# Performance work log

Measured on AMD Instinct MI355X. Metric: run time of the kernel, lower is better.

The kernel has to match this reference:

```python
import jax, jax.numpy as jnp
import numpy as np
from jax.scipy.special import erf, digamma, i0

B, L, D, H = 4, 4096, 512, 4
_MAX_SQRT_GRADIENT = 1000.0

@jax.custom_vjp
def sqrt_bound(x):
    return jnp.sqrt(x)

def _sb_fwd(x):
    return jnp.sqrt(x), x

def _sb_bwd(x, g):
    return (g / jnp.sqrt(jnp.clip(4.0 * x, 1.0 / _MAX_SQRT_GRADIENT**2, None)),)

sqrt_bound.defvjp(_sb_fwd, _sb_bwd)

def block_diag_linear(x, w):
    # x: [..., D], w: [h, bw, bw] block-diagonal weight
    h, bw, _ = w.shape
    xr = x.reshape(x.shape[:-1] + (h, bw))
    return jnp.einsum('...hi,hij->...hj', xr, w).reshape(x.shape)

def self_att_pool(x, num_heads):
    n_state = x.shape[-1] // num_heads
    attn = jax.nn.softmax(jnp.einsum('bld,bmd->blm', x, x) / np.float32(np.sqrt(n_state)), axis=-1)
    # max over the sequence axis of the attended values, keepdims -> [B,1,D]
    return jnp.max(jnp.einsum('blm,bmd->bld', attn, x), axis=-2, keepdims=True)

def ripple_transform_hybrid(t, mix_params):
    mix = jax.nn.softmax(mix_params)
    return mix[0] * digamma(t + 1.0) + mix[1] * i0(t)

def ripple_act(data, alpha, beta, mix_params, temperature=1.0):
    def f(d):
        norm = erf(d / (jnp.max(d) * alpha))
        return jnp.sum(ripple_transform_hybrid(norm * beta, mix_params))
    g = jnp.clip(jax.grad(f)(data), -1.0, 1.0)
    return jax.nn.softmax(-g / temperature, axis=-1)  # softmin

def ripplemoe_act(data, weights, alphas, beta, mix_params, temperature=1.0):
    def f(d):
        dmax = jnp.max(d)
        norm = erf(d[None] / (dmax * alphas[:, None, None]))  # [S,B,L]
        t = ripple_transform_hybrid(norm * beta, mix_params)
        w = jax.nn.softmax(weights)
        return jnp.sum(w[:, None, None] * t)
    g = jnp.clip(jax.grad(f)(data), -1.0, 1.0)
    return jax.nn.softmax(-g / temperature, axis=-1)  # softmin

def token_selection(x, cls_w, cls_b, token_weights, prelu_a, ts_weights, ts_alphas, ts_beta, ts_mix):
    scores = jnp.einsum('bld,sd->sbl', x, cls_w) + cls_b[:, None, None]  # [S,B,L]
    p = jnp.where(scores >= 0, scores, prelu_a * scores)  # PReLU
    ts = jax.nn.celu(p) * jax.nn.silu(p) + jax.nn.gelu(p, approximate=False)
    combined = jnp.einsum('s,sbl->bl', jax.nn.selu(token_weights[:, 0]), ts)
    _, idx = jax.lax.top_k(combined, combined.shape[-1])  # k = L, descending permutation
    vals = ts.sum(0)  # [B,L]
    b_idx = jnp.arange(combined.shape[0])[:, None]
    importance = jnp.ones_like(combined).at[b_idx, idx].add(vals)
    return (1.0 + ripplemoe_act(importance, ts_weights, ts_alphas, ts_beta, ts_mix))[..., None]

def _forward(x, attention_space, W_spatial, W_sil, W_ohead, W_out, w_ig, w_ag, a_param,
             cls_w, cls_b, token_weights, prelu_a, ts_weights, ts_alphas, ts_beta, ts_mix,
             pa1_alpha, pa1_beta, pa1_mix, pa2_alpha, pa2_beta, pa2_mix):
    spatial = jnp.einsum('bld,de->ble', x, attention_space) @ W_spatial.T
    # RG-LRU style gating
    gate_x = jax.nn.sigmoid(block_diag_linear(x, w_ig))
    gate_a = jax.nn.sigmoid(block_diag_linear(x, w_ag))
    log_a = -8.0 * jax.nn.softplus(a_param) * gate_a
    normalized_x = x * gate_x * sqrt_bound(1.0 - jnp.exp(2.0 * log_a))
    gated = jnp.exp(log_a) * self_att_pool(spatial, H) + normalized_x
    sparsity = ripple_act(gated @ W_sil.T, pa1_alpha, pa1_beta, pa1_mix)
    attn = (gated * sparsity) @ W_ohead.T
    sel = token_selection(x, cls_w, cls_b, token_weights, prelu_a, ts_weights, ts_alphas, ts_beta, ts_mix)
    out = ripple_act(attn * sel, pa2_alpha, pa2_beta, pa2_mix)
    return out @ W_out.T

def setup_inputs() -> dict:
    key = jax.random.key(0)
    ks = jax.random.split(key, 12)
    lim = float(1.0 / np.sqrt(D))
    xav = float(np.sqrt(6.0 / (2 * D)))
    bw = D // H
    u = jax.random.uniform(ks[8], (D,), jnp.float32, 0.9**2 + 1e-8, 0.999**2 + 1e-8)
    return {
        'x': jax.random.normal(ks[0], (B, L, D), jnp.float32),
        'attention_space': jax.random.uniform(ks[1], (D, D), jnp.float32, -xav, xav),
        'W_spatial': jax.random.uniform(ks[2], (D, D), jnp.float32, -lim, lim),
        'W_sil': jax.random.uniform(ks[3], (D, D), jnp.float32, -lim, lim),
        'W_ohead': jax.random.uniform(ks[4], (D, D), jnp.float32, -lim, lim),
        'W_out': jax.random.uniform(ks[5], (D, D), jnp.float32, -lim, lim),
        'w_ig': jax.random.normal(ks[6], (H, bw, bw), jnp.float32) * np.float32(np.sqrt(1.0 / bw)),
        'w_ag': jax.random.normal(ks[7], (H, bw, bw), jnp.float32) * np.float32(np.sqrt(1.0 / bw)),
        'a_param': jnp.log(jnp.exp(-0.5 * jnp.log(u)) - 1.0),
        'cls_w': jax.random.uniform(ks[9], (H, D), jnp.float32, -lim, lim),
        'cls_b': jax.random.uniform(ks[10], (H,), jnp.float32, -lim, lim),
        'token_weights': jax.random.normal(ks[11], (H, 1), jnp.float32),
        'prelu_a': jnp.array(0.25, jnp.float32),
        'ts_weights': jnp.ones(H, jnp.float32) / H,
        'ts_alphas': jnp.ones(H, jnp.float32),
        'ts_beta': jnp.array(1.0, jnp.float32),
        'ts_mix': jnp.full((2,), 0.5, jnp.float32),
        'pa1_alpha': jnp.array(1.0, jnp.float32),
        'pa1_beta': jnp.array(1.0, jnp.float32),
        'pa1_mix': jnp.full((2,), 0.5, jnp.float32),
        'pa2_alpha': jnp.array(1.0, jnp.float32),
        'pa2_beta': jnp.array(1.0, jnp.float32),
        'pa2_mix': jnp.full((2,), 0.5, jnp.float32),
    }

def reference(x, attention_space, W_spatial, W_sil, W_ohead, W_out, w_ig, w_ag, a_param,
              cls_w, cls_b, token_weights, prelu_a, ts_weights, ts_alphas, ts_beta, ts_mix,
              pa1_alpha, pa1_beta, pa1_mix, pa2_alpha, pa2_beta, pa2_mix):
    return _forward(x, attention_space, W_spatial, W_sil, W_ohead, W_out, w_ig, w_ag, a_param,
                    cls_w, cls_b, token_weights, prelu_a, ts_weights, ts_alphas, ts_beta, ts_mix,
                    pa1_alpha, pa1_beta, pa1_mix, pa2_alpha, pa2_beta, pa2_mix)
```

## Files before the change

kernel.cpp:

```cpp
#include <hip/hip_runtime.h>

typedef unsigned short ushort;
typedef unsigned int uint;
typedef unsigned long long u64;

#define DEV __device__ __forceinline__

typedef __attribute__((ext_vector_type(4))) float f32x4;
typedef __bf16 bf16x8 __attribute__((ext_vector_type(8)));
typedef __attribute__((ext_vector_type(4))) ushort u16x4;
typedef __attribute__((ext_vector_type(8))) ushort u16x8;

static constexpr int B_ = 4, L_ = 4096, D_ = 512;
static constexpr long NE = (long)B_ * L_ * D_;

DEV float b2f(ushort u) { return __uint_as_float(((uint)u) << 16); }
DEV ushort f2b(float f) {
    uint u = __float_as_uint(f);
    uint r = u + 0x7FFFu + ((u >> 16) & 1u);
    return (ushort)(r >> 16);
}
DEV uint mapF(float f) {
    uint b = __float_as_uint(f);
    return (b & 0x80000000u) ? ~b : (b | 0x80000000u);
}
DEV float unmapF(uint u) {
    uint b = (u & 0x80000000u) ? (u & 0x7FFFFFFFu) : ~u;
    return __uint_as_float(b);
}
DEV float rcp_(float x) { return __builtin_amdgcn_rcpf(x); }
DEV float fexp(float x) { return __builtin_amdgcn_exp2f(x * 1.44269504089f); }
DEV float sigm(float x) { return rcp_(1.f + fexp(-x)); }

DEV void gload16(const ushort* g, ushort* l) {
    __builtin_amdgcn_global_load_lds((const __attribute__((address_space(1))) void*)g,
                                     (__attribute__((address_space(3))) void*)l, 16, 0, 0);
}

DEV int xcd_swz(int b, int nwg) {
    int q = nwg >> 3, r = nwg & 7;
    int x = b & 7, i = b >> 3;
    int base = (x < r) ? x * (q + 1) : r * (q + 1) + (x - r) * q;
    return base + i;
}

DEV float trigamma1p(float t) {
    float x = t + 1.f;
    float acc = 0.f;
#pragma unroll
    for (int k = 0; k < 6; k++) { float xx = x + (float)k; acc += rcp_(xx * xx); }
    float y = x + 6.f;
    float iy = rcp_(y), iy2 = iy * iy;
    return acc + iy * (1.f + iy * (0.5f + iy * (0.166666667f + iy2 * (-0.0333333333f + iy2 * 0.0238095238f))));
}
DEV float besselI1(float t) {
    float q = 0.25f * t * t;
    return 0.5f * t * (1.f + q * (0.5f + q * (0.0833333333f + q * (0.00694444444f + q * (3.47222222e-4f + q * 1.15740741e-5f)))));
}
DEV float rippleH(float u, float beta, float mix0, float mix1) {
    float t = beta * erff(u);
    float Tp = mix0 * trigamma1p(t) + mix1 * besselI1(t);
    float ep = 1.12837917f * fexp(-u * u);
    return beta * Tp * ep;
}

DEV void gemm_core(const ushort* __restrict__ A, int lda,
                   const ushort* __restrict__ Bt, int ldb, int K,
                   ushort* __restrict__ Alds, ushort* __restrict__ Blds,
                   f32x4 (&acc)[4][4])
{
    const int tid = threadIdx.x;
    const int lane = tid & 63;
    const int wave = tid >> 6;
    const int wr = wave >> 1, wc = wave & 1;

    const int srow = wave * 16 + (lane >> 2);
    const int skc = (lane & 3) * 8;
    const ushort* Ag0 = A + (size_t)srow * lda + skc;
    const ushort* Ag1 = A + (size_t)(srow + 64) * lda + skc;
    const ushort* Bg0 = Bt + (size_t)srow * ldb + skc;
    const ushort* Bg1 = Bt + (size_t)(srow + 64) * ldb + skc;
    const int wb = wave * 512;

    const int ar = wr * 64 + (lane & 15);
    const int br = wc * 64 + (lane & 15);
    const int kk = (lane >> 4) * 8;

    gload16(Ag0, Alds + wb);
    gload16(Ag1, Alds + 2048 + wb);
    gload16(Bg0, Blds + wb);
    gload16(Bg1, Blds + 2048 + wb);
    __syncthreads();

    int cur = 0;
    for (int k0 = 0; k0 < K; k0 += 32) {
        const int nb = cur ^ 1;
        if (k0 + 32 < K) {
            gload16(Ag0 + k0 + 32, Alds + nb * 4096 + wb);
            gload16(Ag1 + k0 + 32, Alds + nb * 4096 + 2048 + wb);
            gload16(Bg0 + k0 + 32, Blds + nb * 4096 + wb);
            gload16(Bg1 + k0 + 32, Blds + nb * 4096 + 2048 + wb);
        }
        bf16x8 af[4], bfr[4];
#pragma unroll
        for (int mi = 0; mi < 4; mi++) af[mi] = *(const bf16x8*)&Alds[cur * 4096 + (ar + mi * 16) * 32 + kk];
#pragma unroll
        for (int ni = 0; ni < 4; ni++) bfr[ni] = *(const bf16x8*)&Blds[cur * 4096 + (br + ni * 16) * 32 + kk];
#pragma unroll
        for (int mi = 0; mi < 4; mi++)
#pragma unroll
            for (int ni = 0; ni < 4; ni++)
                acc[mi][ni] = __builtin_amdgcn_mfma_f32_16x16x32_bf16(af[mi], bfr[ni], acc[mi][ni], 0, 0, 0);
        __syncthreads();
        cur = nb;
    }
}

template <int MODE, bool DOMAX>
__global__ __launch_bounds__(256, 4) void gemm_bt(
    const ushort* __restrict__ A, int lda,
    const ushort* __restrict__ Bt, int ldb,
    void* __restrict__ Cv, int ldc, int K,
    const float* __restrict__ rowScale, u64* __restrict__ pmax)
{
    __shared__ ushort Alds[2 * 128 * 32];
    __shared__ ushort Blds[2 * 128 * 32];
    const int nwg = gridDim.x * gridDim.y;
    const int s = xcd_swz(blockIdx.y * gridDim.x + blockIdx.x, nwg);
    const int bx = s % gridDim.x, by = s / gridDim.x;
    const int row0 = by * 128, col0 = bx * 128;
    f32x4 acc[4][4] = {};
    gemm_core(A + (size_t)row0 * lda, lda, Bt + (size_t)col0 * ldb, ldb, K, Alds, Blds, acc);

    const int tid = threadIdx.x;
    const int lane = tid & 63;
    const int wave = tid >> 6;
    const int wr = wave >> 1, wc = wave & 1;
    const int ocol = col0 + wc * 64 + (lane & 15);
    u64 lp = 0;
#pragma unroll
    for (int mi = 0; mi < 4; mi++) {
        const int rbase = row0 + wr * 64 + mi * 16 + (lane >> 4) * 4;
#pragma unroll
        for (int j = 0; j < 4; j++) {
            float sc = (MODE == 3) ? rowScale[rbase + j] : 1.f;
#pragma unroll
            for (int ni = 0; ni < 4; ni++) {
                float v = acc[mi][ni][j] * sc;
                int cc = ocol + ni * 16;
                if (MODE == 1) ((ushort*)Cv)[(size_t)(rbase + j) * ldc + cc] = f2b(v);
                else ((float*)Cv)[(size_t)(rbase + j) * ldc + cc] = v;
                if (DOMAX) {
                    uint idx = (uint)((rbase + j) * ldc + cc);
                    u64 p = ((u64)mapF(v) << 32) | (u64)(~idx);
                    lp = (p > lp) ? p : lp;
                }
            }
        }
    }
    if (DOMAX) {
#pragma unroll
        for (int off = 32; off > 0; off >>= 1) {
            u64 o = __shfl_xor(lp, off);
            lp = (o > lp) ? o : lp;
        }
        if (lane == 0) atomicMax(pmax, lp);
    }
}

__global__ __launch_bounds__(512, 1) void gemm256_exp_k(
    const ushort* __restrict__ spP,
    ushort* __restrict__ Sout,
    float* __restrict__ rowsum)
{
    __shared__ ushort Alds[4 * 256 * 32];
    __shared__ ushort Blds[4 * 256 * 32];
    const int z = blockIdx.z;
    const int nwg = gridDim.x * gridDim.y;
    const int s = xcd_swz(blockIdx.y * gridDim.x + blockIdx.x, nwg);
    const int bx = s % gridDim.x, by = s / gridDim.x;
    const int row0 = by * 256, col0 = bx * 256;
    const ushort* A = spP + (size_t)z * (4096 * 512) + (size_t)row0 * 512;
    const ushort* Bt = spP + (size_t)z * (4096 * 512) + (size_t)col0 * 512;

    const int tid = threadIdx.x;
    const int lane = tid & 63;
    const int wave = tid >> 6;
    const int wr = wave >> 2, wc = wave & 3;

    const int srow = wave * 32 + (lane >> 2);
    const int skc = ((lane & 3) ^ ((lane >> 3) & 3)) * 8;
    const ushort* Ag0 = A + (size_t)srow * 512 + skc;
    const ushort* Ag1 = A + (size_t)(srow + 16) * 512 + skc;
    const ushort* Bg0 = Bt + (size_t)srow * 512 + skc;
    const ushort* Bg1 = Bt + (size_t)(srow + 16) * 512 + skc;
    const int wb = wave * 1024;

    const int ar = wr * 128 + (lane & 15);
    const int br = wc * 64 + (lane & 15);
    const int kk = ((lane >> 4) ^ (((lane & 15) >> 1) & 3)) * 8;

    f32x4 acc[8][4] = {};

#define STG(st, bf) do { \
    gload16(Ag0 + (st) * 32, Alds + (bf) * 8192 + wb); \
    gload16(Ag1 + (st) * 32, Alds + (bf) * 8192 + wb + 512); \
    gload16(Bg0 + (st) * 32, Blds + (bf) * 8192 + wb); \
    gload16(Bg1 + (st) * 32, Blds + (bf) * 8192 + wb + 512); } while (0)

    STG(0, 0); STG(1, 1); STG(2, 2);

    for (int k = 0; k < 16; k++) {
        const int cb = k & 3;
        if (k + 3 < 16) STG(k + 3, (k + 3) & 3);
        if (k < 13)       asm volatile("s_waitcnt vmcnt(12)" ::: "memory");
        else if (k == 13) asm volatile("s_waitcnt vmcnt(8)" ::: "memory");
        else if (k == 14) asm volatile("s_waitcnt vmcnt(4)" ::: "memory");
        else              asm volatile("s_waitcnt vmcnt(0)" ::: "memory");
        __builtin_amdgcn_s_barrier();
        asm volatile("" ::: "memory");
        bf16x8 af[8], bfr[4];
#pragma unroll
        for (int mi = 0; mi < 8; mi++) af[mi] = *(const bf16x8*)&Alds[cb * 8192 + (ar + mi * 16) * 32 + kk];
#pragma unroll
        for (int ni = 0; ni < 4; ni++) bfr[ni] = *(const bf16x8*)&Blds[cb * 8192 + (br + ni * 16) * 32 + kk];
#pragma unroll
        for (int mi = 0; mi < 8; mi++)
#pragma unroll
            for (int ni = 0; ni < 4; ni++)
                acc[mi][ni] = __builtin_amdgcn_mfma_f32_16x16x32_bf16(af[mi], bfr[ni], acc[mi][ni], 0, 0, 0);
        asm volatile("s_waitcnt lgkmcnt(0)" ::: "memory");
        __builtin_amdgcn_s_barrier();
        asm volatile("" ::: "memory");
    }
#undef STG

    ushort* C = Sout + (size_t)z * 16777216;
    float* rs = rowsum + z * 4096;
    const float sc128 = 0.0883883476f;
    const int ocol = col0 + wc * 64 + (lane & 15);
#pragma unroll
    for (int mi = 0; mi < 8; mi++) {
        const int rbase = row0 + wr * 128 + mi * 16 + (lane >> 4) * 4;
#pragma unroll
        for (int j = 0; j < 4; j++) {
            float rsum = 0.f;
#pragma unroll
            for (int ni = 0; ni < 4; ni++) {
                float p = fexp(acc[mi][ni][j] * sc128);
                C[(size_t)(rbase + j) * 4096 + ocol + ni * 16] = f2b(p);
                rsum += p;
            }
#pragma unroll
            for (int off = 1; off < 16; off <<= 1) rsum += __shfl_xor(rsum, off);
            if ((lane & 15) == 0) atomicAdd(&rs[rbase + j], rsum);
        }
    }
}

__global__ __launch_bounds__(256, 4) void pv_split_k(const ushort* __restrict__ P, const ushort* __restrict__ Vt,
                                                     float* __restrict__ part)
{
    __shared__ ushort Alds[2 * 128 * 32];
    __shared__ ushort Blds[2 * 128 * 32];
    const int ks = blockIdx.z;
    const int nwg = gridDim.x * gridDim.y;
    const int s = xcd_swz(blockIdx.y * gridDim.x + blockIdx.x, nwg);
    const int bx = s % gridDim.x, by = s / gridDim.x;
    const int row0 = by * 128, col0 = bx * 128;
    f32x4 acc[4][4] = {};
    gemm_core(P + (size_t)row0 * 4096 + ks * 1024, 4096,
              Vt + (size_t)col0 * 4096 + ks * 1024, 4096, 1024, Alds, Blds, acc);

    float* C = part + (size_t)ks * 2097152 + (size_t)row0 * 512 + col0;
    const int tid = threadIdx.x;
    const int lane = tid & 63;
    const int wave = tid >> 6;
    const int wr = wave >> 1, wc = wave & 1;
    const int ocol = wc * 64 + (lane & 15);
#pragma unroll
    for (int mi = 0; mi < 4; mi++) {
        const int rl = wr * 64 + mi * 16 + (lane >> 4) * 4;
#pragma unroll
        for (int j = 0; j < 4; j++)
#pragma unroll
            for (int ni = 0; ni < 4; ni++)
                C[(size_t)(rl + j) * 512 + ocol + ni * 16] = acc[mi][ni][j];
    }
}

__global__ __launch_bounds__(256) void pool_combine_k(const float* __restrict__ part, const float* __restrict__ rs,
                                                      uint* __restrict__ poolU)
{
    const int tid = threadIdx.x;
    const int l0 = blockIdx.x * 32;
    float m0 = -3.4e38f, m1 = -3.4e38f;
    for (int l = 0; l < 32; l++) {
        size_t off = (size_t)(l0 + l) * 512;
        float iv = rcp_(rs[l0 + l]);
        float s0 = 0.f, s1 = 0.f;
#pragma unroll
        for (int ks = 0; ks < 4; ks++) {
            s0 += part[(size_t)ks * 2097152 + off + tid];
            s1 += part[(size_t)ks * 2097152 + off + tid + 256];
        }
        m0 = fmaxf(m0, s0 * iv); m1 = fmaxf(m1, s1 * iv);
    }
    atomicMax(&poolU[tid], mapF(m0));
    atomicMax(&poolU[tid + 256], mapF(m1));
}

__global__ __launch_bounds__(256, 4) void gate_gemm_k(const ushort* __restrict__ xb,
                                                      const ushort* __restrict__ wigT, const ushort* __restrict__ wagT,
                                                      ushort* __restrict__ gxab, ushort* __restrict__ gaab)
{
    __shared__ ushort Alds[2 * 128 * 32];
    __shared__ ushort Blds[2 * 128 * 32];
    const int which = blockIdx.x;
    const int h = blockIdx.z;
    const ushort* A = xb + (size_t)blockIdx.y * 128 * 512 + h * 128;
    const ushort* W = (which ? wagT : wigT) + (size_t)h * 16384;
    f32x4 acc[4][4] = {};
    gemm_core(A, 512, W, 128, 128, Alds, Blds, acc);

    ushort* C = (which ? gaab : gxab) + (size_t)blockIdx.y * 128 * 512 + h * 128;
    const int tid = threadIdx.x;
    const int lane = tid & 63;
    const int wave = tid >> 6;
    const int wr = wave >> 1, wc = wave & 1;
    const int ocol = wc * 64 + (lane & 15);
#pragma unroll
    for (int mi = 0; mi < 4; mi++) {
        const int rl = wr * 64 + mi * 16 + (lane >> 4) * 4;
#pragma unroll
        for (int j = 0; j < 4; j++)
#pragma unroll
            for (int ni = 0; ni < 4; ni++)
                C[(size_t)(rl + j) * 512 + ocol + ni * 16] = f2b(acc[mi][ni][j]);
    }
}

__global__ void convert_f2b_k(const float* __restrict__ s, ushort* __restrict__ d, long n4) {
    long i = (long)blockIdx.x * blockDim.x + threadIdx.x;
    long st = (long)gridDim.x * blockDim.x;
    for (; i < n4; i += st) {
        f32x4 v = ((const f32x4*)s)[i];
        u16x4 o;
        o[0] = f2b(v[0]); o[1] = f2b(v[1]); o[2] = f2b(v[2]); o[3] = f2b(v[3]);
        ((u16x4*)d)[i] = o;
    }
}

__global__ void convert_w4_k(const float* __restrict__ w0, const float* __restrict__ w1,
                             const float* __restrict__ w2, const float* __restrict__ w3,
                             ushort* __restrict__ dst) {
    const float* srcs[4] = {w0, w1, w2, w3};
    const float* s = srcs[blockIdx.y];
    ushort* d = dst + (size_t)blockIdx.y * 262144;
    int i = blockIdx.x * 256 + threadIdx.x;
    f32x4 v = ((const f32x4*)s)[i];
    u16x4 o;
    o[0] = f2b(v[0]); o[1] = f2b(v[1]); o[2] = f2b(v[2]); o[3] = f2b(v[3]);
    ((u16x4*)d)[i] = o;
}

template <bool SRCF32>
__global__ __launch_bounds__(256) void transpose_to_bf16(const void* __restrict__ srcv, ushort* __restrict__ dst, int R, int C) {
    __shared__ float tile[32][33];
    const int z = blockIdx.z;
    const float* sf = (const float*)srcv + (size_t)z * R * C;
    const ushort* sb = (const ushort*)srcv + (size_t)z * R * C;
    ushort* dz = dst + (size_t)z * R * C;
    const int tx = threadIdx.x & 31, ty = threadIdx.x >> 5;
    const int c = blockIdx.x * 32 + tx;
#pragma unroll
    for (int k = 0; k < 4; k++) {
        const int r = blockIdx.y * 32 + ty + k * 8;
        tile[ty + k * 8][tx] = SRCF32 ? sf[(size_t)r * C + c] : b2f(sb[(size_t)r * C + c]);
    }
    __syncthreads();
#pragma unroll
    for (int k = 0; k < 4; k++) {
        const int dr = blockIdx.x * 32 + ty + k * 8;
        const int dc = blockIdx.y * 32 + tx;
        dz[(size_t)dr * R + dc] = f2b(tile[tx][ty + k * 8]);
    }
}

__global__ __launch_bounds__(256) void transpose_gates_k(const float* __restrict__ wig, const float* __restrict__ wag,
                                                         ushort* __restrict__ wigT, ushort* __restrict__ wagT) {
    __shared__ float tile[32][33];
    const int which = blockIdx.z >> 2, h = blockIdx.z & 3;
    const float* src = (which ? wag : wig) + (size_t)h * 16384;
    ushort* dst = (which ? wagT : wigT) + (size_t)h * 16384;
    const int tx = threadIdx.x & 31, ty = threadIdx.x >> 5;
    const int c = blockIdx.x * 32 + tx;
#pragma unroll
    for (int k = 0; k < 4; k++) {
        const int r = blockIdx.y * 32 + ty + k * 8;
        tile[ty + k * 8][tx] = src[(size_t)r * 128 + c];
    }
    __syncthreads();
#pragma unroll
    for (int k = 0; k < 4; k++) {
        const int dr = blockIdx.x * 32 + ty + k * 8;
        const int dc = blockIdx.y * 32 + tx;
        dst[(size_t)dr * 128 + dc] = f2b(tile[tx][ty + k * 8]);
    }
}

__global__ void init_misc_k(uint* poolU, u64* pmax) {
    int i = blockIdx.x * 256 + threadIdx.x;
    if (i < 2048) poolU[i] = 0u;
    if (i < 4) pmax[i] = 0ull;
}
__global__ void zero_rs_k(float* rs) {
    rs[blockIdx.x * 256 + threadIdx.x] = 0.f;
}
__global__ void sentinel_k(float* o) { o[threadIdx.x] = 1.0e6f; }

__global__ __launch_bounds__(256) void gates_gated_k(const float* __restrict__ x, const ushort* __restrict__ gxab,
                                                     const ushort* __restrict__ gaab, const float* __restrict__ a_param,
                                                     const uint* __restrict__ poolU, ushort* __restrict__ gatedb) {
    __shared__ float sp8[512];
    const int tid = threadIdx.x;
    for (int d = tid; d < 512; d += 256) {
        float a = a_param[d];
        sp8[d] = 8.f * (fmaxf(a, 0.f) + log1pf(expf(-fabsf(a))));
    }
    __syncthreads();
    long i = (long)blockIdx.x * blockDim.x + tid;
    long st = (long)gridDim.x * blockDim.x;
    const long n8 = NE >> 3;
    for (; i < n8; i += st) {
        u16x8 gx8 = ((const u16x8*)gxab)[i];
        u16x8 ga8 = ((const u16x8*)gaab)[i];
        f32x4 x0 = ((const f32x4*)x)[2 * i];
        f32x4 x1 = ((const f32x4*)x)[2 * i + 1];
        long e = i << 3;
        int b = (int)(e >> 21);
        int d0 = (int)(e & 511);
        u16x8 o;
#pragma unroll
        for (int j = 0; j < 8; j++) {
            float xv = (j < 4) ? x0[j] : x1[j - 4];
            float gx = sigm(b2f(gx8[j]));
            float ga = sigm(b2f(ga8[j]));
            float la = -sp8[d0 + j] * ga;
            float ea = fexp(la);
            float nx = xv * gx * sqrtf(fmaxf(1.f - fexp(2.f * la), 0.f));
            float pl = unmapF(poolU[b * 512 + d0 + j]);
            o[j] = f2b(ea * pl + nx);
        }
        ((u16x8*)gatedb)[i] = o;
    }
}

__global__ __launch_bounds__(256) void redmax2_k(const float* __restrict__ bmax, const int* __restrict__ bidx, int n,
                                                 float* __restrict__ outM, int* __restrict__ outI) {
    __shared__ float rv[256];
    __shared__ int ri[256];
    const int tid = threadIdx.x;
    float bv = -3.4e38f; int bi = -1;
    for (int i = tid; i < n; i += 256) {
        float v = bmax[i]; int ix = bidx[i];
        if (ix >= 0 && (bi < 0 || v > bv || (v == bv && ix < bi))) { bv = v; bi = ix; }
    }
    rv[tid] = bv; ri[tid] = bi; __syncthreads();
    for (int s = 128; s > 0; s >>= 1) {
        if (tid < s) {
            float ov = rv[tid + s]; int oi = ri[tid + s];
            if (oi >= 0 && (ri[tid] < 0 || ov > rv[tid] || (ov == rv[tid] && oi < ri[tid]))) { rv[tid] = ov; ri[tid] = oi; }
        }
        __syncthreads();
    }
    if (tid == 0) { outM[0] = rv[0]; outI[0] = ri[0]; }
}

__global__ __launch_bounds__(256) void ripple_g_k(const float* __restrict__ d, ushort* __restrict__ gb, float* __restrict__ sspart,
                                                  const u64* __restrict__ pmax, const float* __restrict__ alpha_p,
                                                  const float* __restrict__ beta_p, const float* __restrict__ mix_p) {
    __shared__ float red[256];
    const int tid = threadIdx.x;
    const float M = unmapF((uint)(pmax[0] >> 32));
    const float alpha = alpha_p[0], beta = beta_p[0];
    float m0 = mix_p[0], m1 = mix_p[1];
    float mm = fmaxf(m0, m1);
    float e0 = fexp(m0 - mm), e1 = fexp(m1 - mm);
    float inv = rcp_(e0 + e1);
    float mix0 = e0 * inv, mix1 = e1 * inv;
    const float invMA = rcp_(M * alpha);
    float ss = 0.f;
    long g = (long)blockIdx.x * 256 + tid;
    const long stride = (long)gridDim.x * 256;
    for (long i = g; i < NE; i += stride) {
        float dv = d[i];
        float H = rippleH(dv * invMA, beta, mix0, mix1);
        gb[i] = f2b(H * invMA);
        ss += H * dv;
    }
    red[tid] = ss; __syncthreads();
    for (int s = 128; s > 0; s >>= 1) { if (tid < s) red[tid] += red[tid + s]; __syncthreads(); }
    if (tid == 0) sspart[blockIdx.x] = red[0];
}
__global__ __launch_bounds__(256) void redsum2_k(const float* __restrict__ part, int n, float* __restrict__ out) {
    __shared__ float red[256];
    const int tid = threadIdx.x;
    float s = 0.f;
    for (int i = tid; i < n; i += 256) s += part[i];
    red[tid] = s; __syncthreads();
    for (int q = 128; q > 0; q >>= 1) { if (tid < q) red[tid] += red[tid + q]; __syncthreads(); }
    if (tid == 0) out[0] = red[0];
}

template <int GS>
__global__ __launch_bounds__(256) void ripple_softmax_k(const ushort* __restrict__ gb,
                                                        const u64* __restrict__ pmax,
                                                        const float* __restrict__ ssTot, const float* __restrict__ alpha_p,
                                                        const ushort* __restrict__ gatedb, ushort* __restrict__ outb) {
    __shared__ float red[256];
    const int tid = threadIdx.x;
    const float M = unmapF((uint)(pmax[0] >> 32));
    const int amax = (int)(~(uint)(pmax[0] & 0xFFFFFFFFull));
    const float corr = ssTot[0] * rcp_(M * M * alpha_p[0]);
    long base = (long)blockIdx.x * 512;
    float g0 = b2f(gb[base + tid]);
    float g1 = b2f(gb[base + tid + 256]);
    if ((int)(base + tid) == amax) g0 -= corr;
    if ((int)(base + tid + 256) == amax) g1 -= corr;
    g0 = fminf(fmaxf(g0, -1.f), 1.f);
    g1 = fminf(fmaxf(g1, -1.f), 1.f);
    float mn = fminf(g0, g1);
    red[tid] = mn; __syncthreads();
    for (int s = 128; s > 0; s >>= 1) { if (tid < s) red[tid] = fminf(red[tid], red[tid + s]); __syncthreads(); }
    mn = red[0]; __syncthreads();
    float e0 = fexp(mn - g0), e1 = fexp(mn - g1);
    red[tid] = e0 + e1; __syncthreads();
    for (int s = 128; s > 0; s >>= 1) { if (tid < s) red[tid] += red[tid + s]; __syncthreads(); }
    float inv = rcp_(red[0]);
    if (GS) {
        outb[base + tid] = f2b(b2f(gatedb[base + tid]) * (e0 * inv));
        outb[base + tid + 256] = f2b(b2f(gatedb[base + tid + 256]) * (e1 * inv));
    } else {
        outb[base + tid] = f2b(e0 * inv);
        outb[base + tid + 256] = f2b(e1 * inv);
    }
}

__global__ __launch_bounds__(256) void ts1_k(const float* __restrict__ x, const float* __restrict__ cls_w,
                                             const float* __restrict__ cls_b, const float* __restrict__ tw,
                                             const float* __restrict__ prelu_a,
                                             float* __restrict__ combined, float* __restrict__ vals) {
    __shared__ float cw[2048];
    const int tid = threadIdx.x;
    for (int i = tid; i < 2048; i += 256) cw[i] = cls_w[i];
    __syncthreads();
    const int lane = tid & 63, wid = tid >> 6;
    const int row = blockIdx.x * 4 + wid;
    const float* xr = x + (size_t)row * 512 + lane * 8;
    float pa0 = 0, pa1 = 0, pa2 = 0, pa3 = 0;
#pragma unroll
    for (int j = 0; j < 8; j++) {
        float v = xr[j];
        int c = lane * 8 + j;
        pa0 += v * cw[c]; pa1 += v * cw[512 + c]; pa2 += v * cw[1024 + c]; pa3 += v * cw[1536 + c];
    }
#pragma unroll
    for (int o = 32; o > 0; o >>= 1) {
        pa0 += __shfl_down(pa0, o); pa1 += __shfl_down(pa1, o);
        pa2 += __shfl_down(pa2, o); pa3 += __shfl_down(pa3, o);
    }
    if (lane == 0) {
        float a = prelu_a[0];
        float sc[4] = {pa0, pa1, pa2, pa3};
        float comb = 0.f, vsum = 0.f;
#pragma unroll
        for (int s = 0; s < 4; s++) {
            float p = sc[s] + cls_b[s];
            p = (p >= 0.f) ? p : a * p;
            float cel = (p > 0.f) ? p : expm1f(p);
            float sil = p * sigm(p);
            float gel = 0.5f * p * (1.f + erff(p * 0.70710678f));
            float ts = cel * sil + gel;
            float ww = tw[s];
            float se = 1.05070099f * ((ww > 0.f) ? ww : 1.67326324f * expm1f(ww));
            comb += se * ts;
            vsum += ts;
        }
        combined[row] = comb;
        vals[row] = vsum;
    }
}

__global__ __launch_bounds__(256) void ts2a_k(const float* __restrict__ combined, int* __restrict__ rankp) {
    __shared__ float q[512];
    const int b = blockIdx.z;
    const int tid = threadIdx.x;
    const float* cr = combined + b * 4096;
    const int q0 = blockIdx.y * 512;
    for (int i = tid; i < 512; i += 256) q[i] = cr[q0 + i];
    __syncthreads();
    const int p = blockIdx.x * 256 + tid;
    const float cp = cr[p];
    const f32x4* q4 = (const f32x4*)q;
    int rank = 0;
#pragma unroll 8
    for (int i4 = 0; i4 < 128; i4++) {
        f32x4 v = q4[i4];
        int qb = q0 + i4 * 4;
        rank += (v[0] > cp) || (v[0] == cp && (qb + 0) < p);
        rank += (v[1] > cp) || (v[1] == cp && (qb + 1) < p);
        rank += (v[2] > cp) || (v[2] == cp && (qb + 2) < p);
        rank += (v[3] > cp) || (v[3] == cp && (qb + 3) < p);
    }
    rankp[((b * 8 + blockIdx.y) * 4096) + p] = rank;
}

__global__ __launch_bounds__(256) void ts2b_k(const int* __restrict__ rankp, const float* __restrict__ vals,
                                              float* __restrict__ imp, float* __restrict__ bmax, int* __restrict__ bidx) {
    __shared__ float rv[256];
    __shared__ int ri[256];
    const int tid = threadIdx.x;
    const int b = blockIdx.y;
    const int p = blockIdx.x * 256 + tid;
    int rank = 0;
#pragma unroll
    for (int c = 0; c < 8; c++) rank += rankp[((b * 8 + c) * 4096) + p];
    const int gi = b * 4096 + p;
    const float v = 1.f + vals[b * 4096 + rank];
    imp[gi] = v;
    rv[tid] = v; ri[tid] = gi; __syncthreads();
    for (int s = 128; s > 0; s >>= 1) {
        if (tid < s) {
            float ov = rv[tid + s]; int oi = ri[tid + s];
            if (ov > rv[tid] || (ov == rv[tid] && oi < ri[tid])) { rv[tid] = ov; ri[tid] = oi; }
        }
        __syncthreads();
    }
    if (tid == 0) { bmax[b * 16 + blockIdx.x] = rv[0]; bidx[b * 16 + blockIdx.x] = ri[0]; }
}

__global__ __launch_bounds__(256) void moe_g_k(const float* __restrict__ imp, float* __restrict__ gmoe,
                                               float* __restrict__ sspart, const float* __restrict__ scalM,
                                               const float* __restrict__ tsw, const float* __restrict__ tsa,
                                               const float* __restrict__ tsb, const float* __restrict__ tsmix) {
    __shared__ float red[256];
    const int tid = threadIdx.x;
    const float M = scalM[0];
    float w[4], invMA[4], invA[4];
    {
        float wm = fmaxf(fmaxf(tsw[0], tsw[1]), fmaxf(tsw[2], tsw[3]));
        float s = 0.f;
#pragma unroll
        for (int k = 0; k < 4; k++) { w[k] = fexp(tsw[k] - wm); s += w[k]; }
        float si = rcp_(s);
#pragma unroll
        for (int k = 0; k < 4; k++) { w[k] *= si; invMA[k] = rcp_(M * tsa[k]); invA[k] = rcp_(tsa[k]); }
    }
    const float beta = tsb[0];
    float m0 = tsmix[0], m1 = tsmix[1];
    float mm = fmaxf(m0, m1);
    float e0 = fexp(m0 - mm), e1 = fexp(m1 - mm);
    float minv = rcp_(e0 + e1);
    const float mix0 = e0 * minv, mix1 = e1 * minv;

    float ss = 0.f;
    int i = blockIdx.x * 256 + tid;
    const int stride = gridDim.x * 256;
    for (; i < 65536; i += stride) {
        float dv = imp[i];
        float gbv = 0.f;
#pragma unroll
        for (int s = 0; s < 4; s++) {
            float H = rippleH(dv * invMA[s], beta, mix0, mix1);
            gbv += w[s] * H * invMA[s];
            ss += w[s] * H * dv * invA[s];
        }
        gmoe[i] = gbv;
    }
    red[tid] = ss; __syncthreads();
    for (int s = 128; s > 0; s >>= 1) { if (tid < s) red[tid] += red[tid + s]; __syncthreads(); }
    if (tid == 0) sspart[blockIdx.x] = red[0];
}

__global__ __launch_bounds__(256) void moe_sel_k(const float* __restrict__ gmoe, const float* __restrict__ scalM,
                                                 const int* __restrict__ scalI, const float* __restrict__ sspart,
                                                 float* __restrict__ sel) {
    __shared__ float red[256];
    const int tid = threadIdx.x;
    const int b = blockIdx.x;
    const float M = scalM[0];
    const int amax = scalI[0];
    float ssTot = 0.f;
#pragma unroll
    for (int k = 0; k < 64; k++) ssTot += sspart[k];
    const float corr = ssTot * rcp_(M * M);
    float g[16];
    float mn = 3.4e38f;
#pragma unroll
    for (int k = 0; k < 16; k++) {
        int i = b * 4096 + tid + k * 256;
        float v = gmoe[i];
        if (i == amax) v -= corr;
        v = fminf(fmaxf(v, -1.f), 1.f);
        g[k] = v;
        mn = fminf(mn, v);
    }
    red[tid] = mn; __syncthreads();
    for (int s = 128; s > 0; s >>= 1) { if (tid < s) red[tid] = fminf(red[tid], red[tid + s]); __syncthreads(); }
    mn = red[0]; __syncthreads();
    float sum = 0.f;
#pragma unroll
    for (int k = 0; k < 16; k++) { g[k] = fexp(mn - g[k]); sum += g[k]; }
    red[tid] = sum; __syncthreads();
    for (int s = 128; s > 0; s >>= 1) { if (tid < s) red[tid] += red[tid + s]; __syncthreads(); }
    float inv = rcp_(red[0]);
#pragma unroll
    for (int k = 0; k < 16; k++) sel[b * 4096 + tid + k * 256] = 1.f + g[k] * inv;
}

static constexpr size_t OFF_XB    = 0;
static constexpr size_t OFF_TMPB  = 16777216;
static constexpr size_t OFF_SPB   = 33554432;
static constexpr size_t OFF_SPT   = 50331648;
static constexpr size_t OFF_DBUF  = 67108864;
static constexpr size_t OFF_HBUF  = 100663296;
static constexpr size_t OFF_GATB  = 134217728;
static constexpr size_t OFF_NXB   = 150994944;
static constexpr size_t OFF_EAB   = 167772160;
static constexpr size_t OFF_AST   = 184549376;
static constexpr size_t OFF_WSP   = 185073664;
static constexpr size_t OFF_WSIL  = 185597952;
static constexpr size_t OFF_WOH   = 186122240;
static constexpr size_t OFF_WOUT  = 186646528;
static constexpr size_t OFF_WIGT  = 187170816;
static constexpr size_t OFF_WAGT  = 187301888;
static constexpr size_t OFF_POOL  = 187432960;
static constexpr size_t OFF_SCAL  = 187441152;
static constexpr size_t OFF_SCALI = 187441408;
static constexpr size_t OFF_BMAX  = 187441664;
static constexpr size_t OFF_BIDX  = 187449856;
static constexpr size_t OFF_SSP   = 187458048;
static constexpr size_t OFF_COMB  = 187466240;
static constexpr size_t OFF_VALS  = 187728384;
static constexpr size_t OFF_IMP   = 187990528;
static constexpr size_t OFF_GMOE  = 188252672;
static constexpr size_t OFF_SEL   = 188514816;
static constexpr size_t WS_NEED   = 188776960;

extern "C" void kernel_launch(void* const* d_in, const int* in_sizes, int n_in,
                              void* d_out, int out_size, void* d_ws, size_t ws_size,
                              hipStream_t stream)
{
    (void)in_sizes; (void)n_in; (void)out_size;
    const float* x    = (const float*)d_in[0];
    const float* AS   = (const float*)d_in[1];
    const float* Wsp  = (const float*)d_in[2];
    const float* Wsil = (const float*)d_in[3];
    const float* Woh  = (const float*)d_in[4];
    const float* Wout = (const float*)d_in[5];
    const float* wig  = (const float*)d_in[6];
    const float* wag  = (const float*)d_in[7];
    const float* a_param = (const float*)d_in[8];
    const float* cls_w = (const float*)d_in[9];
    const float* cls_b = (const float*)d_in[10];
    const float* tokw  = (const float*)d_in[11];
    const float* prelu = (const float*)d_in[12];
    const float* tsw   = (const float*)d_in[13];
    const float* tsa   = (const float*)d_in[14];
    const float* tsb   = (const float*)d_in[15];
    const float* tsmix = (const float*)d_in[16];
    const float* p1a = (const float*)d_in[17];
    const float* p1b = (const float*)d_in[18];
    const float* p1m = (const float*)d_in[19];
    const float* p2a = (const float*)d_in[20];
    const float* p2b = (const float*)d_in[21];
    const float* p2m = (const float*)d_in[22];
    float* out = (float*)d_out;

    char* w = (char*)d_ws;
    if (ws_size < WS_NEED) { sentinel_k<<<1, 256, 0, stream>>>(out); return; }

    ushort* xb    = (ushort*)(w + OFF_XB);
    ushort* tmpb  = (ushort*)(w + OFF_TMPB);
    ushort* spb   = (ushort*)(w + OFF_SPB);
    ushort* spT   = (ushort*)(w + OFF_SPT);
    float*  dbuf  = (float*)(w + OFF_DBUF);
    ushort* gbb   = (ushort*)(w + OFF_HBUF);
    ushort* Spair = (ushort*)(w + OFF_DBUF);
    float*  pvpart= (float*)(w + OFF_XB);
    int*    rankp = (int*)(w + OFF_DBUF);
    ushort* gatedb= (ushort*)(w + OFF_GATB);
    ushort* gxab  = (ushort*)(w + OFF_NXB);
    ushort* gaab  = (ushort*)(w + OFF_EAB);
    ushort* ASt   = (ushort*)(w + OFF_AST);
    ushort* Wspb  = (ushort*)(w + OFF_WSP);
    ushort* Wsilb = (ushort*)(w + OFF_WSIL);
    ushort* Wohb  = (ushort*)(w + OFF_WOH);
    ushort* Woutb = (ushort*)(w + OFF_WOUT);
    ushort* wigT  = (ushort*)(w + OFF_WIGT);
    ushort* wagT  = (ushort*)(w + OFF_WAGT);
    uint*   poolU = (uint*)(w + OFF_POOL);
    float*  scal  = (float*)(w + OFF_SCAL);
    u64*    pmax  = (u64*)(w + OFF_SCAL + 128);
    int*    scalI = (int*)(w + OFF_SCALI);
    float*  bmax  = (float*)(w + OFF_BMAX);
    int*    bidx  = (int*)(w + OFF_BIDX);
    float*  sspart= (float*)(w + OFF_SSP);
    float*  comb  = (float*)(w + OFF_COMB);
    float*  rowsum= comb;
    float*  vals  = (float*)(w + OFF_VALS);
    float*  imp   = (float*)(w + OFF_IMP);
    float*  gmoe  = (float*)(w + OFF_GMOE);
    float*  sel   = (float*)(w + OFF_SEL);
    ushort* gsb     = tmpb;
    ushort* probs2b = xb;

    convert_f2b_k<<<2048, 256, 0, stream>>>(x, xb, NE >> 2);
    convert_w4_k<<<dim3(256, 4), 256, 0, stream>>>(Wsp, Wsil, Woh, Wout, Wspb);
    transpose_to_bf16<true><<<dim3(16, 16, 1), 256, 0, stream>>>(AS, ASt, 512, 512);
    transpose_gates_k<<<dim3(4, 4, 8), 256, 0, stream>>>(wig, wag, wigT, wagT);
    init_misc_k<<<8, 256, 0, stream>>>(poolU, pmax);

    gate_gemm_k<<<dim3(2, 128, 4), 256, 0, stream>>>(xb, wigT, wagT, gxab, gaab);

    gemm_bt<1, false><<<dim3(4, 128), 256, 0, stream>>>(xb, 512, ASt, 512, tmpb, 512, 512, nullptr, nullptr);
    gemm_bt<1, false><<<dim3(4, 128), 256, 0, stream>>>(tmpb, 512, Wspb, 512, spb, 512, 512, nullptr, nullptr);

    transpose_to_bf16<false><<<dim3(16, 128, 4), 256, 0, stream>>>(spb, spT, 4096, 512);
    for (int p = 0; p < 2; p++) {
        const ushort* spP = spb + (size_t)(2 * p) * L_ * D_;
        zero_rs_k<<<32, 256, 0, stream>>>(rowsum);
        gemm256_exp_k<<<dim3(16, 16, 2), 512, 0, stream>>>(spP, Spair, rowsum);
        for (int z = 0; z < 2; z++) {
            const int b = 2 * p + z;
            pv_split_k<<<dim3(4, 32, 4), 256, 0, stream>>>(Spair + (size_t)z * 16777216,
                                                           spT + (size_t)b * D_ * L_, pvpart);
            pool_combine_k<<<128, 256, 0, stream>>>(pvpart, rowsum + z * 4096, poolU + b * 512);
        }
    }

    gates_gated_k<<<1024, 256, 0, stream>>>(x, gxab, gaab, a_param, poolU, gatedb);

    gemm_bt<0, true><<<dim3(4, 128), 256, 0, stream>>>(gatedb, 512, Wsilb, 512, dbuf, 512, 512, nullptr, &pmax[0]);
    ripple_g_k<<<2048, 256, 0, stream>>>(dbuf, gbb, sspart, &pmax[0], p1a, p1b, p1m);
    redsum2_k<<<1, 256, 0, stream>>>(sspart, 2048, &scal[1]);
    ripple_softmax_k<1><<<16384, 256, 0, stream>>>(gbb, &pmax[0], &scal[1], p1a, gatedb, gsb);

    ts1_k<<<4096, 256, 0, stream>>>(x, cls_w, cls_b, tokw, prelu, comb, vals);
    ts2a_k<<<dim3(16, 8, 4), 256, 0, stream>>>(comb, rankp);
    ts2b_k<<<dim3(16, 4), 256, 0, stream>>>(rankp, vals, imp, bmax, bidx);
    redmax2_k<<<1, 256, 0, stream>>>(bmax, bidx, 64, &scal[4], &scalI[2]);
    moe_g_k<<<64, 256, 0, stream>>>(imp, gmoe, sspart, &scal[4], tsw, tsa, tsb, tsmix);
    moe_sel_k<<<4, 256, 0, stream>>>(gmoe, &scal[4], &scalI[2], sspart, sel);

    gemm_bt<3, true><<<dim3(4, 128), 256, 0, stream>>>(gsb, 512, Wohb, 512, dbuf, 512, 512, sel, &pmax[1]);

    ripple_g_k<<<2048, 256, 0, stream>>>(dbuf, gbb, sspart, &pmax[1], p2a, p2b, p2m);
    redsum2_k<<<1, 256, 0, stream>>>(sspart, 2048, &scal[3]);
    ripple_softmax_k<0><<<16384, 256, 0, stream>>>(gbb, &pmax[1], &scal[3], p2a, nullptr, probs2b);

    gemm_bt<0, false><<<dim3(4, 128), 256, 0, stream>>>(probs2b, 512, Woutb, 512, out, 512, 512, nullptr, nullptr);
}
```

Measured before the change: 625.9 us.

## Switch score GEMM to 64-wide K tiles with double buffering and setprio

Restructures the LDS staging of the 256x256 score GEMM. It moves from a 4-deep ring of 32-wide K slices to a 2-deep ring of 64-wide K slices, using a new XOR swizzle over 8 chunks. This halves the number of barrier round-trips per tile and raises MFMA priority with s_setprio during compute. The trade-off is shallower prefetch, with one stage in flight instead of three, so more of the global load latency may be exposed.

```diff
diff --git a/kernel.cpp b/kernel.cpp
--- a/kernel.cpp
+++ b/kernel.cpp
@@ -173,8 +173,8 @@
     ushort* __restrict__ Sout,
     float* __restrict__ rowsum)
 {
-    __shared__ ushort Alds[4 * 256 * 32];
-    __shared__ ushort Blds[4 * 256 * 32];
+    __shared__ ushort Alds[2 * 256 * 64];
+    __shared__ ushort Blds[2 * 256 * 64];
     const int z = blockIdx.z;
     const int nwg = gridDim.x * gridDim.y;
     const int s = xcd_swz(blockIdx.y * gridDim.x + blockIdx.x, nwg);
@@ -188,47 +188,49 @@
     const int wave = tid >> 6;
     const int wr = wave >> 2, wc = wave & 3;
 
-    const int srow = wave * 32 + (lane >> 2);
-    const int skc = ((lane & 3) ^ ((lane >> 3) & 3)) * 8;
-    const ushort* Ag0 = A + (size_t)srow * 512 + skc;
-    const ushort* Ag1 = A + (size_t)(srow + 16) * 512 + skc;
-    const ushort* Bg0 = Bt + (size_t)srow * 512 + skc;
-    const ushort* Bg1 = Bt + (size_t)(srow + 16) * 512 + skc;
-    const int wb = wave * 1024;
+    const int lrow = lane >> 3;
+    const int lchunk = (lane & 7) ^ lrow;
+    const ushort* Asrc = A + (size_t)(wave * 32 + lrow) * 512 + lchunk * 8;
+    const ushort* Bsrc = Bt + (size_t)(wave * 32 + lrow) * 512 + lchunk * 8;
+    const int wlds = wave * 2048;
 
     const int ar = wr * 128 + (lane & 15);
     const int br = wc * 64 + (lane & 15);
-    const int kk = ((lane >> 4) ^ (((lane & 15) >> 1) & 3)) * 8;
 
     f32x4 acc[8][4] = {};
 
-#define STG(st, bf) do { \
-    gload16(Ag0 + (st) * 32, Alds + (bf) * 8192 + wb); \
-    gload16(Ag1 + (st) * 32, Alds + (bf) * 8192 + wb + 512); \
-    gload16(Bg0 + (st) * 32, Blds + (bf) * 8192 + wb); \
-    gload16(Bg1 + (st) * 32, Blds + (bf) * 8192 + wb + 512); } while (0)
-
-    STG(0, 0); STG(1, 1); STG(2, 2);
-
-    for (int k = 0; k < 16; k++) {
-        const int cb = k & 3;
-        if (k + 3 < 16) STG(k + 3, (k + 3) & 3);
-        if (k < 13)       asm volatile("s_waitcnt vmcnt(12)" ::: "memory");
-        else if (k == 13) asm volatile("s_waitcnt vmcnt(8)" ::: "memory");
-        else if (k == 14) asm volatile("s_waitcnt vmcnt(4)" ::: "memory");
-        else              asm volatile("s_waitcnt vmcnt(0)" ::: "memory");
+#define STG(kt, bf) do { \
+    _Pragma("unroll") \
+    for (int c = 0; c < 4; c++) { \
+        gload16(Asrc + (size_t)c * 8 * 512 + (kt) * 64, Alds + (bf) * 16384 + wlds + c * 512); \
+        gload16(Bsrc + (size_t)c * 8 * 512 + (kt) * 64, Blds + (bf) * 16384 + wlds + c * 512); \
+    } } while (0)
+
+    STG(0, 0);
+
+    for (int kt = 0; kt < 8; kt++) {
+        const int cb = kt & 1;
+        if (kt < 7) STG(kt + 1, cb ^ 1);
+        if (kt < 7) asm volatile("s_waitcnt vmcnt(8)" ::: "memory");
+        else        asm volatile("s_waitcnt vmcnt(0)" ::: "memory");
         __builtin_amdgcn_s_barrier();
         asm volatile("" ::: "memory");
-        bf16x8 af[8], bfr[4];
-#pragma unroll
-        for (int mi = 0; mi < 8; mi++) af[mi] = *(const bf16x8*)&Alds[cb * 8192 + (ar + mi * 16) * 32 + kk];
-#pragma unroll
-        for (int ni = 0; ni < 4; ni++) bfr[ni] = *(const bf16x8*)&Blds[cb * 8192 + (br + ni * 16) * 32 + kk];
-#pragma unroll
-        for (int mi = 0; mi < 8; mi++)
-#pragma unroll
-            for (int ni = 0; ni < 4; ni++)
-                acc[mi][ni] = __builtin_amdgcn_mfma_f32_16x16x32_bf16(af[mi], bfr[ni], acc[mi][ni], 0, 0, 0);
+        __builtin_amdgcn_s_setprio(1);
+#pragma unroll
+        for (int ks = 0; ks < 2; ks++) {
+            const int kc = ((ks * 4 + (lane >> 4)) ^ (lane & 7)) * 8;
+            bf16x8 af[8], bfr[4];
+#pragma unroll
+            for (int mi = 0; mi < 8; mi++) af[mi] = *(const bf16x8*)&Alds[cb * 16384 + (ar + mi * 16) * 64 + kc];
+#pragma unroll
+            for (int ni = 0; ni < 4; ni++) bfr[ni] = *(const bf16x8*)&Blds[cb * 16384 + (br + ni * 16) * 64 + kc];
+#pragma unroll
+            for (int mi = 0; mi < 8; mi++)
+#pragma unroll
+                for (int ni = 0; ni < 4; ni++)
+                    acc[mi][ni] = __builtin_amdgcn_mfma_f32_16x16x32_bf16(af[mi], bfr[ni], acc[mi][ni], 0, 0, 0);
+        }
+        __builtin_amdgcn_s_setprio(0);
         asm volatile("s_waitcnt lgkmcnt(0)" ::: "memory");
         __builtin_amdgcn_s_barrier();
         asm volatile("" ::: "memory");
```

After: 625.7 us. No clear change (-0.0%).
